# Optimization experiments

Measured on AMD Instinct MI355X. Metric: run time of the kernel, lower is better.

Reference implementation:

```python
import jax, jax.numpy as jnp
import numpy as np

NSAMPLES = [64, 32, 16, 8, 4]
TEMPERATURE = 1.0


def square_distance(src, dst):
    # src [B,N,C], dst [B,M,C] -> [B,N,M]
    d = -2.0 * jnp.einsum('bnc,bmc->bnm', src, dst)
    d = d + jnp.sum(src ** 2, -1)[:, :, None]
    d = d + jnp.sum(dst ** 2, -1)[:, None, :]
    return d


def knn_point(nsample, xyz, new_xyz):
    # indices of nsample nearest points in xyz for each query in new_xyz
    sqrdists = square_distance(new_xyz, xyz)           # [B,S,N]
    _, idx = jax.lax.top_k(-sqrdists, nsample)         # smallest distances
    return idx                                         # [B,S,nsample]


def index_points(points, idx):
    # points [B,N,C], idx [B,S,K] -> [B,S,K,C]
    B, S, K = idx.shape
    flat = idx.reshape(B, S * K)
    out = jnp.take_along_axis(points, flat[..., None], axis=1)
    return out.reshape(B, S, K, points.shape[-1])


def boundary_loss(labels, coords, feats, num_classes):
    onehot = jax.nn.one_hot(labels, num_classes, dtype=jnp.float32)  # [B,N,C]
    loss = jnp.float32(0.0)
    for i, (coord, feat) in enumerate(zip(coords, feats)):
        if i == 0:
            probability_labels = onehot
        else:
            kneighbors = i * 4
            nb_idx = knn_point(kneighbors, coords[0], coord)          # [B,Ni,k]
            probability_labels = index_points(onehot, nb_idx).mean(-2)  # [B,Ni,C]
        nsample = NSAMPLES[i]
        neighbor_indexs = knn_point(nsample, coord, coord)            # [B,Ni,ns]
        neighbor_labels = index_points(probability_labels, neighbor_indexs)  # [B,Ni,ns,C]
        neighbor_feats = index_points(feat, neighbor_indexs)          # [B,Ni,ns,D]
        center_label = jnp.argmax(probability_labels, -1)[:, :, None]  # [B,Ni,1]
        neighbor_label = jnp.argmax(neighbor_labels, -1)               # [B,Ni,ns]
        mask = (center_label == neighbor_label)                        # [B,Ni,ns] bool
        cnt = jnp.sum(mask.astype(jnp.int32), -1)
        point_mask = (cnt > 0) & (cnt < nsample)                       # [B,Ni]
        any_pm = jnp.any(point_mask)
        pm = point_mask.astype(jnp.float32)[:, :, None]                # [B,Ni,1]
        # pairwise feature distances to the nsample neighbors
        diff = feat[:, :, None, :] - neighbor_feats                    # [B,Ni,ns,D]
        dist = jnp.sqrt(jnp.sum(diff ** 2, -1) + 1e-6)                 # [B,Ni,ns]
        dist = -dist
        dist = dist - jnp.max(dist, -1, keepdims=True)
        dist = dist / TEMPERATURE
        exp = jnp.exp(dist)
        pos = jnp.sum(exp * mask.astype(jnp.float32) * pm)
        neg = jnp.sum(exp * pm)
        pos = jnp.where(any_pm, pos, 1.0)
        neg = jnp.where(any_pm, neg, 1.0)
        term = -jnp.log(pos / (neg + 1e-6))
        loss = loss + jnp.where(any_pm, term, 0.0)
    return loss


def setup_inputs() -> dict:
    key = jax.random.key(0)
    ks = jax.random.split(key, 12)
    B, N = 2, 4096
    sizes = [N, N // 4, N // 16, N // 64, N // 256]
    inp = {}
    inp['labels'] = jax.random.randint(ks[0], (B, N), 0, 21)
    for i, s in enumerate(sizes):
        inp[f'coord{i}'] = jax.random.normal(ks[1 + i], (B, s, 3), dtype=jnp.float32)
        inp[f'feat{i}'] = jax.random.normal(ks[6 + i], (B, s, 32), dtype=jnp.float32)
    inp['num_classes'] = 21
    return inp


def reference(labels, coord0, coord1, coord2, coord3, coord4,
              feat0, feat1, feat2, feat3, feat4, num_classes):
    coords = [coord0, coord1, coord2, coord3, coord4]
    feats = [feat0, feat1, feat2, feat3, feat4]
    return boundary_loss(labels, coords, feats, num_classes)
```

## Files before the change

kernel.cpp:

```cpp
#include <hip/hip_runtime.h>
#include <math.h>

#define WAVE 64
#define NC 21

__device__ __forceinline__ unsigned f32_ord(float f) {
    unsigned u = __float_as_uint(f);
    return (u & 0x80000000u) ? ~u : (u | 0x80000000u);
}

__device__ __forceinline__ int wave_red_sum_dpp(int v) {
    v += __builtin_amdgcn_update_dpp(0, v, 0x111, 0xf, 0xf, true);
    v += __builtin_amdgcn_update_dpp(0, v, 0x112, 0xf, 0xf, true);
    v += __builtin_amdgcn_update_dpp(0, v, 0x114, 0xf, 0xf, true);
    v += __builtin_amdgcn_update_dpp(0, v, 0x118, 0xf, 0xf, true);
    v += __builtin_amdgcn_update_dpp(0, v, 0x142, 0xa, 0xf, true);
    v += __builtin_amdgcn_update_dpp(0, v, 0x143, 0xc, 0xf, true);
    return __builtin_amdgcn_readlane(v, 63);
}

__device__ __forceinline__ unsigned wave_min_u32(unsigned v) {
#pragma unroll
    for (int off = 32; off >= 1; off >>= 1) {
        unsigned o = (unsigned)__shfl_xor((int)v, off, WAVE);
        v = (o < v) ? o : v;
    }
    return v;
}

__device__ __forceinline__ unsigned wave_max_u32(unsigned v) {
#pragma unroll
    for (int off = 32; off >= 1; off >>= 1) {
        unsigned o = (unsigned)__shfl_xor((int)v, off, WAVE);
        v = (o > v) ? o : v;
    }
    return v;
}

__device__ __forceinline__ float wave_max_f32(float v) {
#pragma unroll
    for (int off = 32; off >= 1; off >>= 1)
        v = fmaxf(v, __shfl_xor(v, off, WAVE));
    return v;
}

__device__ __forceinline__ float wave_sum_f32(float v) {
#pragma unroll
    for (int off = 32; off >= 1; off >>= 1)
        v += __shfl_xor(v, off, WAVE);
    return v;
}

struct SelShm {
    unsigned long long cand[512];
    int wcnt[4];
    int sel[64];
};

template <int NI, int NS>
__device__ __forceinline__ void block_select_topNS(
    const float* __restrict__ rp,
    float qx, float qy, float qz, float nq,
    SelShm& shm, int tid)
{
    constexpr int SLICE = NI / 4;
    constexpr int NPL = (SLICE >= 64) ? (SLICE / 64) : 1;
    constexpr int CAPX = (NS < 32) ? 32 : NS;
    constexpr int STRIDE = NS + CAPX;
    const int lane = tid & 63;
    const int wid = tid >> 6;
    const int wbase = wid * SLICE;
    const unsigned long long lmask = (1ull << lane) - 1ull;

    unsigned ok[NPL];
#pragma unroll
    for (int j = 0; j < NPL; ++j) {
        unsigned o = 0xFFFFFFFFu;
        int gl = (SLICE >= 64) ? (j * 64 + lane) : lane;
        if (SLICE >= 64 || lane < SLICE) {
            int g = wbase + gl;
            float rx = rp[3*g], ry = rp[3*g+1], rz = rp[3*g+2];
            float nr = rx*rx + ry*ry + rz*rz;
            float dot = qx*rx + qy*ry + qz*rz;
            o = f32_ord(-2.0f*dot + nq + nr);
        }
        ok[j] = o;
    }

    unsigned mn = 0xFFFFFFFFu, mx = 0u;
#pragma unroll
    for (int j = 0; j < NPL; ++j) {
        mn = (ok[j] < mn) ? ok[j] : mn;
        unsigned v = (ok[j] == 0xFFFFFFFFu) ? 0u : ok[j];
        mx = (v > mx) ? v : mx;
    }
    mn = wave_min_u32(mn);
    mx = wave_max_u32(mx);

    unsigned lo = mn, hi = mx;
    int cLo = 0, cHi = SLICE;
    while (lo < hi && (cHi - cLo) > CAPX) {
        unsigned piv = lo + ((hi - lo) >> 1);
        int c = 0;
#pragma unroll
        for (int j = 0; j < NPL; ++j) c += (ok[j] <= piv) ? 1 : 0;
        c = wave_red_sum_dpp(c);
        if (c >= NS) { hi = piv; cHi = c; } else { lo = piv + 1; cLo = c; }
    }

    unsigned long long* cw = shm.cand + wid * STRIDE;
    int wcnt;
    if (lo == hi && (cHi - cLo) > CAPX) {
        unsigned V = lo;
        int off = 0;
#pragma unroll
        for (int j = 0; j < NPL; ++j) {
            bool s = ok[j] < V;
            unsigned long long mk = __ballot(s);
            if (s) {
                int gl = (SLICE >= 64) ? (j*64 + lane) : lane;
                cw[off + __popcll(mk & lmask)] =
                    ((unsigned long long)ok[j] << 32) | (unsigned)(wbase + gl);
            }
            off += __popcll(mk);
        }
        int R = NS - off;
        unsigned consumed = 0u;
        for (int r = 0; r < R; ++r) {
            int bj = -1;
#pragma unroll
            for (int j = NPL - 1; j >= 0; --j)
                if (ok[j] == V && !((consumed >> j) & 1u)) bj = j;
            unsigned g = 0xFFFFFFFFu;
            if (bj >= 0) {
                int gl = (SLICE >= 64) ? (bj*64 + lane) : lane;
                g = (unsigned)(wbase + gl);
            }
            unsigned mg = wave_min_u32(g);
            if (bj >= 0 && g == mg) consumed |= (1u << bj);
            if (lane == 0) cw[off + r] = ((unsigned long long)V << 32) | mg;
        }
        wcnt = NS;
    } else {
        int off = 0;
#pragma unroll
        for (int j = 0; j < NPL; ++j) {
            bool s = ok[j] <= hi;
            unsigned long long mk = __ballot(s);
            if (s) {
                int gl = (SLICE >= 64) ? (j*64 + lane) : lane;
                cw[off + __popcll(mk & lmask)] =
                    ((unsigned long long)ok[j] << 32) | (unsigned)(wbase + gl);
            }
            off += __popcll(mk);
        }
        wcnt = off;
    }
    if (lane == 0) shm.wcnt[wid] = wcnt;
    __syncthreads();

    if (wid == 0) {
        constexpr int CAND = 4 * STRIDE;
        constexpr int NPLC = (CAND + 63) / 64;
        unsigned long long ck[NPLC];
        int w0 = shm.wcnt[0], w1 = shm.wcnt[1], w2 = shm.wcnt[2], w3 = shm.wcnt[3];
#pragma unroll
        for (int i = 0; i < NPLC; ++i) {
            int idx = i * 64 + lane;
            unsigned long long v = ~0ull;
            if (idx < CAND) {
                int w = idx / STRIDE;
                int slot = idx - w * STRIDE;
                int wc = (w == 0) ? w0 : (w == 1) ? w1 : (w == 2) ? w2 : w3;
                if (slot < wc) v = shm.cand[idx];
            }
            ck[i] = v;
        }
        unsigned mn2 = 0xFFFFFFFFu, mx2 = 0u;
#pragma unroll
        for (int i = 0; i < NPLC; ++i) {
            unsigned k = (unsigned)(ck[i] >> 32);
            mn2 = (k < mn2) ? k : mn2;
            unsigned v = (k == 0xFFFFFFFFu) ? 0u : k;
            mx2 = (v > mx2) ? v : mx2;
        }
        mn2 = wave_min_u32(mn2);
        mx2 = wave_max_u32(mx2);
        unsigned lo2 = mn2, hi2 = mx2;
        while (lo2 < hi2) {
            unsigned piv = lo2 + ((hi2 - lo2) >> 1);
            int c = 0;
#pragma unroll
            for (int i = 0; i < NPLC; ++i)
                c += ((unsigned)(ck[i] >> 32) <= piv) ? 1 : 0;
            c = wave_red_sum_dpp(c);
            if (c >= NS) hi2 = piv; else lo2 = piv + 1;
        }
        unsigned V2 = lo2;
        int c2 = 0;
#pragma unroll
        for (int i = 0; i < NPLC; ++i)
            c2 += ((unsigned)(ck[i] >> 32) < V2) ? 1 : 0;
        int clt2 = wave_red_sum_dpp(c2);
        int R2 = NS - clt2;
        int off = 0;
#pragma unroll
        for (int i = 0; i < NPLC; ++i) {
            bool s = ((unsigned)(ck[i] >> 32)) < V2;
            unsigned long long mk = __ballot(s);
            if (s) shm.sel[off + __popcll(mk & lmask)] = (int)(unsigned)ck[i];
            off += __popcll(mk);
        }
        unsigned consumed = 0u;
        for (int r = 0; r < R2; ++r) {
            unsigned bg = 0xFFFFFFFFu; int bi = -1;
#pragma unroll
            for (int i = 0; i < NPLC; ++i) {
                unsigned k = (unsigned)(ck[i] >> 32);
                unsigned g = (unsigned)ck[i];
                if (k == V2 && !((consumed >> i) & 1u) && g < bg) { bg = g; bi = i; }
            }
            unsigned mg = wave_min_u32(bg);
            if (bi >= 0 && bg == mg) consumed |= (1u << bi);
            if (lane == 0) shm.sel[clt2 + r] = (int)mg;
        }
    }
}

template <int NQ, int K>
__device__ __forceinline__ void knn_level(
    const float* __restrict__ qc, const float* __restrict__ rc,
    const int* __restrict__ rl, int* __restrict__ out,
    int qb, SelShm& shm, int tid)
{
    int b = qb / NQ, qi = qb - b * NQ;
    const float* qp = qc + ((long)b * NQ + qi) * 3;
    float qx = qp[0], qy = qp[1], qz = qp[2];
    float nq = qx*qx + qy*qy + qz*qz;
    block_select_topNS<4096, K>(rc + (long)b * 4096 * 3, qx, qy, qz, nq, shm, tid);
    if ((tid >> 6) == 0) {
        int lane = tid & 63;
        int lb = (lane < K) ? rl[(long)b * 4096 + shm.sel[lane]] : -1;
        int cnt = 0;
#pragma unroll
        for (int k = 0; k < K; ++k) {
            int lk = __shfl(lb, k, WAVE);
            cnt += (lk == lane) ? 1 : 0;
        }
        int key = (lane < NC) ? ((cnt << 8) | (255 - lane)) : 0;
#pragma unroll
        for (int off = 32; off >= 1; off >>= 1) {
            int o = __shfl_xor(key, off, WAVE);
            key = (o > key) ? o : key;
        }
        if (lane == 0) out[(long)b * NQ + qi] = 255 - (key & 255);
    }
}

template <int NI, int NS>
__device__ __forceinline__ void boundary_level(
    const float* __restrict__ coord, const float* __restrict__ feat,
    const int* __restrict__ lbl,
    double* __restrict__ pos, double* __restrict__ neg, int* __restrict__ anyf,
    int qb, SelShm& shm, int tid)
{
    int b = qb / NI, qi = qb - b * NI;
    const float* qp = coord + ((long)b * NI + qi) * 3;
    float qx = qp[0], qy = qp[1], qz = qp[2];
    float nq = qx*qx + qy*qy + qz*qz;
    block_select_topNS<NI, NS>(coord + (long)b * NI * 3, qx, qy, qz, nq, shm, tid);
    if ((tid >> 6) == 0) {
        int lane = tid & 63;
        int center = lbl[(long)b * NI + qi];
        bool m = false;
        float dj = -INFINITY;
        if (lane < NS) {
            int nb = shm.sel[lane];
            m = (lbl[(long)b * NI + nb] == center);
            const float4* fq = (const float4*)(feat + ((long)b * NI + qi) * 32);
            const float4* fn = (const float4*)(feat + ((long)b * NI + nb) * 32);
            float s = 0.f;
#pragma unroll
            for (int d = 0; d < 8; ++d) {
                float4 a = fq[d], c = fn[d];
                float d0 = a.x - c.x, d1 = a.y - c.y;
                float d2 = a.z - c.z, d3 = a.w - c.w;
                s += d0*d0 + d1*d1 + d2*d2 + d3*d3;
            }
            dj = -sqrtf(s + 1e-6f);
        }
        unsigned long long mb = __ballot(m);
        int cnt = __popcll(mb);
        float mxv = wave_max_f32(dj);
        float ej = 0.f, pj = 0.f;
        if (lane < NS) {
            ej = expf(dj - mxv);
            pj = m ? ej : 0.f;
        }
        float se = wave_sum_f32(ej);
        float sp = wave_sum_f32(pj);
        bool pm = (cnt > 0) && (cnt < NS);
        if (pm && lane == 0) {
            atomicAdd(pos, (double)sp);
            atomicAdd(neg, (double)se);
            *anyf = 1;
        }
    }
}

__global__ __launch_bounds__(256) void knn_fused(
    const float* __restrict__ c1, const float* __restrict__ c2,
    const float* __restrict__ c3, const float* __restrict__ c4,
    const float* __restrict__ c0, const int* __restrict__ labels,
    int* __restrict__ lbl1, int* __restrict__ lbl2,
    int* __restrict__ lbl3, int* __restrict__ lbl4,
    double* __restrict__ posA, double* __restrict__ negA,
    int* __restrict__ anyA, int B)
{
    __shared__ SelShm shm;
    int blk = blockIdx.x, tid = threadIdx.x;
    int n1 = B * 1024, n2 = n1 + B * 256, n3 = n2 + B * 64, n4 = n3 + B * 16;
    if (blk < n1)      knn_level<1024, 4>(c1, c0, labels, lbl1, blk,      shm, tid);
    else if (blk < n2) knn_level<256,  8>(c2, c0, labels, lbl2, blk - n1, shm, tid);
    else if (blk < n3) knn_level<64,  12>(c3, c0, labels, lbl3, blk - n2, shm, tid);
    else if (blk < n4) knn_level<16,  16>(c4, c0, labels, lbl4, blk - n3, shm, tid);
    else if (tid < 5) { posA[tid] = 0.0; negA[tid] = 0.0; anyA[tid] = 0; }
}

__global__ __launch_bounds__(256) void boundary_fused(
    const float* __restrict__ c0, const float* __restrict__ c1,
    const float* __restrict__ c2, const float* __restrict__ c3,
    const float* __restrict__ c4,
    const float* __restrict__ f0, const float* __restrict__ f1,
    const float* __restrict__ f2, const float* __restrict__ f3,
    const float* __restrict__ f4,
    const int* __restrict__ labels, const int* __restrict__ lbl1,
    const int* __restrict__ lbl2, const int* __restrict__ lbl3,
    const int* __restrict__ lbl4,
    double* __restrict__ posA, double* __restrict__ negA,
    int* __restrict__ anyA, int B)
{
    __shared__ SelShm shm;
    int blk = blockIdx.x, tid = threadIdx.x;
    int m0 = B * 4096, m1 = m0 + B * 1024, m2 = m1 + B * 256;
    int m3 = m2 + B * 64, m4 = m3 + B * 16;
    if (blk < m0)
        boundary_level<4096, 64>(c0, f0, labels, posA+0, negA+0, anyA+0, blk,      shm, tid);
    else if (blk < m1)
        boundary_level<1024, 32>(c1, f1, lbl1,   posA+1, negA+1, anyA+1, blk - m0, shm, tid);
    else if (blk < m2)
        boundary_level<256,  16>(c2, f2, lbl2,   posA+2, negA+2, anyA+2, blk - m1, shm, tid);
    else if (blk < m3)
        boundary_level<64,    8>(c3, f3, lbl3,   posA+3, negA+3, anyA+3, blk - m2, shm, tid);
    else if (blk < m4)
        boundary_level<16,    4>(c4, f4, lbl4,   posA+4, negA+4, anyA+4, blk - m3, shm, tid);
}

__global__ void finalize_kernel(const double* __restrict__ pos,
                                const double* __restrict__ neg,
                                const int* __restrict__ anyf,
                                float* __restrict__ out) {
    if (threadIdx.x == 0 && blockIdx.x == 0) {
        float loss = 0.f;
        for (int i = 0; i < 5; ++i) {
            if (anyf[i]) {
                float p = (float)pos[i];
                float n = (float)neg[i];
                loss += -logf(p / (n + 1e-6f));
            }
        }
        out[0] = loss;
    }
}

extern "C" void kernel_launch(void* const* d_in, const int* in_sizes, int n_in,
                              void* d_out, int out_size, void* d_ws, size_t ws_size,
                              hipStream_t stream) {
    (void)out_size; (void)ws_size;
    const int* labels = (const int*)d_in[0];
    const float* coord[5];
    const float* feat[5];
    bool interleaved = (n_in >= 3 && in_sizes[2] == 2 * 4096 * 32);
    if (interleaved) {
        for (int i = 0; i < 5; ++i) {
            coord[i] = (const float*)d_in[1 + 2 * i];
            feat[i]  = (const float*)d_in[2 + 2 * i];
        }
    } else {
        for (int i = 0; i < 5; ++i) {
            coord[i] = (const float*)d_in[1 + i];
            feat[i]  = (const float*)d_in[6 + i];
        }
    }
    int B = in_sizes[0] / 4096;

    double* posA = (double*)d_ws;
    double* negA = posA + 5;
    int* anyA = (int*)(negA + 5);
    int* lbl1 = anyA + 8;
    int* lbl2 = lbl1 + B * 1024;
    int* lbl3 = lbl2 + B * 256;
    int* lbl4 = lbl3 + B * 64;

    int knn_grid = B * (1024 + 256 + 64 + 16) + 1;
    hipLaunchKernelGGL(knn_fused, dim3(knn_grid), dim3(256), 0, stream,
                       coord[1], coord[2], coord[3], coord[4],
                       coord[0], labels, lbl1, lbl2, lbl3, lbl4,
                       posA, negA, anyA, B);

    int bnd_grid = B * (4096 + 1024 + 256 + 64 + 16);
    hipLaunchKernelGGL(boundary_fused, dim3(bnd_grid), dim3(256), 0, stream,
                       coord[0], coord[1], coord[2], coord[3], coord[4],
                       feat[0], feat[1], feat[2], feat[3], feat[4],
                       labels, lbl1, lbl2, lbl3, lbl4,
                       posA, negA, anyA, B);

    hipLaunchKernelGGL(finalize_kernel, dim3(1), dim3(1), 0, stream,
                       posA, negA, anyA, (float*)d_out);
}
```

Baseline: 391.6 us.

## Replace bisection top-k selection with 4-pass radix histogram select

The per-wave bisection on distance keys followed by a second candidate-merge pass in one wave is replaced with a block-wide 8-bit radix select. Each pass builds shared-memory histograms with atomics, and one wave scans them to find the k-th key. Selected indices are then written with an atomic counter, and ties are broken with a block-wide min loop. This removes the serial bisection iterations and the single-wave merge stage. In exchange it adds LDS atomics, several __syncthreads per pass, and a per-tie block barrier loop.

```diff
diff --git a/kernel.cpp b/kernel.cpp
--- a/kernel.cpp
+++ b/kernel.cpp
@@ -9,16 +9,6 @@
     return (u & 0x80000000u) ? ~u : (u | 0x80000000u);
 }
 
-__device__ __forceinline__ int wave_red_sum_dpp(int v) {
-    v += __builtin_amdgcn_update_dpp(0, v, 0x111, 0xf, 0xf, true);
-    v += __builtin_amdgcn_update_dpp(0, v, 0x112, 0xf, 0xf, true);
-    v += __builtin_amdgcn_update_dpp(0, v, 0x114, 0xf, 0xf, true);
-    v += __builtin_amdgcn_update_dpp(0, v, 0x118, 0xf, 0xf, true);
-    v += __builtin_amdgcn_update_dpp(0, v, 0x142, 0xa, 0xf, true);
-    v += __builtin_amdgcn_update_dpp(0, v, 0x143, 0xc, 0xf, true);
-    return __builtin_amdgcn_readlane(v, 63);
-}
-
 __device__ __forceinline__ unsigned wave_min_u32(unsigned v) {
 #pragma unroll
     for (int off = 32; off >= 1; off >>= 1) {
@@ -28,15 +18,6 @@
     return v;
 }
 
-__device__ __forceinline__ unsigned wave_max_u32(unsigned v) {
-#pragma unroll
-    for (int off = 32; off >= 1; off >>= 1) {
-        unsigned o = (unsigned)__shfl_xor((int)v, off, WAVE);
-        v = (o > v) ? o : v;
-    }
-    return v;
-}
-
 __device__ __forceinline__ float wave_max_f32(float v) {
 #pragma unroll
     for (int off = 32; off >= 1; off >>= 1)
@@ -52,10 +33,42 @@
 }
 
 struct SelShm {
-    unsigned long long cand[512];
-    int wcnt[4];
+    int hist[4][256];
     int sel[64];
+    int swave[4];
+    int scnt;
 };
+
+__device__ __forceinline__ void radix_scan_step(SelShm& shm, int lane,
+                                                int& need, unsigned& Vhi) {
+    int i0 = 4 * lane;
+    int b0 = shm.hist[0][i0]   + shm.hist[1][i0]   + shm.hist[2][i0]   + shm.hist[3][i0];
+    int b1 = shm.hist[0][i0+1] + shm.hist[1][i0+1] + shm.hist[2][i0+1] + shm.hist[3][i0+1];
+    int b2 = shm.hist[0][i0+2] + shm.hist[1][i0+2] + shm.hist[2][i0+2] + shm.hist[3][i0+2];
+    int b3 = shm.hist[0][i0+3] + shm.hist[1][i0+3] + shm.hist[2][i0+3] + shm.hist[3][i0+3];
+    int lsum = b0 + b1 + b2 + b3;
+    int c = lsum;
+#pragma unroll
+    for (int off = 1; off < 64; off <<= 1) {
+        int o = __shfl_up(c, off, WAVE);
+        c += (lane >= off) ? o : 0;
+    }
+    unsigned long long mball = __ballot(c >= need);
+    int Ls = __ffsll((unsigned long long)mball) - 1;
+    int cL = __shfl(c, Ls, WAVE);
+    int lsumL = __shfl(lsum, Ls, WAVE);
+    int B0 = __shfl(b0, Ls, WAVE);
+    int B1 = __shfl(b1, Ls, WAVE);
+    int B2 = __shfl(b2, Ls, WAVE);
+    int e = cL - lsumL;
+    int T;
+    if (e + B0 >= need)                { T = 4 * Ls + 0; }
+    else if (e + B0 + B1 >= need)      { T = 4 * Ls + 1; e += B0; }
+    else if (e + B0 + B1 + B2 >= need) { T = 4 * Ls + 2; e += B0 + B1; }
+    else                               { T = 4 * Ls + 3; e += B0 + B1 + B2; }
+    need -= e;
+    Vhi = (Vhi << 8) | (unsigned)T;
+}
 
 template <int NI, int NS>
 __device__ __forceinline__ void block_select_topNS(
@@ -63,22 +76,18 @@
     float qx, float qy, float qz, float nq,
     SelShm& shm, int tid)
 {
-    constexpr int SLICE = NI / 4;
-    constexpr int NPL = (SLICE >= 64) ? (SLICE / 64) : 1;
-    constexpr int CAPX = (NS < 32) ? 32 : NS;
-    constexpr int STRIDE = NS + CAPX;
+    constexpr int NPL = (NI + 255) / 256;
+    constexpr bool FULL = (NPL * 256 == NI);
     const int lane = tid & 63;
     const int wid = tid >> 6;
-    const int wbase = wid * SLICE;
     const unsigned long long lmask = (1ull << lane) - 1ull;
 
     unsigned ok[NPL];
 #pragma unroll
     for (int j = 0; j < NPL; ++j) {
+        int g = j * 256 + tid;
         unsigned o = 0xFFFFFFFFu;
-        int gl = (SLICE >= 64) ? (j * 64 + lane) : lane;
-        if (SLICE >= 64 || lane < SLICE) {
-            int g = wbase + gl;
+        if (FULL || g < NI) {
             float rx = rp[3*g], ry = rp[3*g+1], rz = rp[3*g+2];
             float nr = rx*rx + ry*ry + rz*rz;
             float dot = qx*rx + qy*ry + qz*rz;
@@ -87,143 +96,78 @@
         ok[j] = o;
     }
 
-    unsigned mn = 0xFFFFFFFFu, mx = 0u;
+    int* hf = &shm.hist[0][0];
+#pragma unroll
+    for (int i = 0; i < 4; ++i) hf[i * 256 + tid] = 0;
+    if (tid == 0) shm.scnt = 0;
+    __syncthreads();
+
+    int need = NS;
+    unsigned Vhi = 0;
+
+#pragma unroll
+    for (int j = 0; j < NPL; ++j)
+        atomicAdd(&shm.hist[wid][ok[j] >> 24], 1);
+    __syncthreads();
+    radix_scan_step(shm, lane, need, Vhi);
+    __syncthreads();
+#pragma unroll
+    for (int i = 0; i < 4; ++i) hf[i * 256 + tid] = 0;
+    __syncthreads();
+
+#pragma unroll
+    for (int pass = 1; pass < 4; ++pass) {
+        const int shift = 24 - 8 * pass;
+#pragma unroll
+        for (int j = 0; j < NPL; ++j) {
+            if ((ok[j] >> (shift + 8)) == Vhi)
+                atomicAdd(&shm.hist[wid][(ok[j] >> shift) & 255], 1);
+        }
+        __syncthreads();
+        radix_scan_step(shm, lane, need, Vhi);
+        __syncthreads();
+        if (pass < 3) {
+#pragma unroll
+            for (int i = 0; i < 4; ++i) hf[i * 256 + tid] = 0;
+            __syncthreads();
+        }
+    }
+
+    const unsigned V = Vhi;
+    const int R = need;
+    const int clt = NS - R;
+
 #pragma unroll
     for (int j = 0; j < NPL; ++j) {
-        mn = (ok[j] < mn) ? ok[j] : mn;
-        unsigned v = (ok[j] == 0xFFFFFFFFu) ? 0u : ok[j];
-        mx = (v > mx) ? v : mx;
-    }
-    mn = wave_min_u32(mn);
-    mx = wave_max_u32(mx);
-
-    unsigned lo = mn, hi = mx;
-    int cLo = 0, cHi = SLICE;
-    while (lo < hi && (cHi - cLo) > CAPX) {
-        unsigned piv = lo + ((hi - lo) >> 1);
-        int c = 0;
-#pragma unroll
-        for (int j = 0; j < NPL; ++j) c += (ok[j] <= piv) ? 1 : 0;
-        c = wave_red_sum_dpp(c);
-        if (c >= NS) { hi = piv; cHi = c; } else { lo = piv + 1; cLo = c; }
-    }
-
-    unsigned long long* cw = shm.cand + wid * STRIDE;
-    int wcnt;
-    if (lo == hi && (cHi - cLo) > CAPX) {
-        unsigned V = lo;
-        int off = 0;
-#pragma unroll
-        for (int j = 0; j < NPL; ++j) {
-            bool s = ok[j] < V;
-            unsigned long long mk = __ballot(s);
-            if (s) {
-                int gl = (SLICE >= 64) ? (j*64 + lane) : lane;
-                cw[off + __popcll(mk & lmask)] =
-                    ((unsigned long long)ok[j] << 32) | (unsigned)(wbase + gl);
-            }
-            off += __popcll(mk);
-        }
-        int R = NS - off;
-        unsigned consumed = 0u;
-        for (int r = 0; r < R; ++r) {
-            int bj = -1;
-#pragma unroll
-            for (int j = NPL - 1; j >= 0; --j)
-                if (ok[j] == V && !((consumed >> j) & 1u)) bj = j;
-            unsigned g = 0xFFFFFFFFu;
-            if (bj >= 0) {
-                int gl = (SLICE >= 64) ? (bj*64 + lane) : lane;
-                g = (unsigned)(wbase + gl);
-            }
-            unsigned mg = wave_min_u32(g);
-            if (bj >= 0 && g == mg) consumed |= (1u << bj);
-            if (lane == 0) cw[off + r] = ((unsigned long long)V << 32) | mg;
-        }
-        wcnt = NS;
-    } else {
-        int off = 0;
-#pragma unroll
-        for (int j = 0; j < NPL; ++j) {
-            bool s = ok[j] <= hi;
-            unsigned long long mk = __ballot(s);
-            if (s) {
-                int gl = (SLICE >= 64) ? (j*64 + lane) : lane;
-                cw[off + __popcll(mk & lmask)] =
-                    ((unsigned long long)ok[j] << 32) | (unsigned)(wbase + gl);
-            }
-            off += __popcll(mk);
-        }
-        wcnt = off;
-    }
-    if (lane == 0) shm.wcnt[wid] = wcnt;
-    __syncthreads();
-
-    if (wid == 0) {
-        constexpr int CAND = 4 * STRIDE;
-        constexpr int NPLC = (CAND + 63) / 64;
-        unsigned long long ck[NPLC];
-        int w0 = shm.wcnt[0], w1 = shm.wcnt[1], w2 = shm.wcnt[2], w3 = shm.wcnt[3];
-#pragma unroll
-        for (int i = 0; i < NPLC; ++i) {
-            int idx = i * 64 + lane;
-            unsigned long long v = ~0ull;
-            if (idx < CAND) {
-                int w = idx / STRIDE;
-                int slot = idx - w * STRIDE;
-                int wc = (w == 0) ? w0 : (w == 1) ? w1 : (w == 2) ? w2 : w3;
-                if (slot < wc) v = shm.cand[idx];
-            }
-            ck[i] = v;
-        }
-        unsigned mn2 = 0xFFFFFFFFu, mx2 = 0u;
-#pragma unroll
-        for (int i = 0; i < NPLC; ++i) {
-            unsigned k = (unsigned)(ck[i] >> 32);
-            mn2 = (k < mn2) ? k : mn2;
-            unsigned v = (k == 0xFFFFFFFFu) ? 0u : k;
-            mx2 = (v > mx2) ? v : mx2;
-        }
-        mn2 = wave_min_u32(mn2);
-        mx2 = wave_max_u32(mx2);
-        unsigned lo2 = mn2, hi2 = mx2;
-        while (lo2 < hi2) {
-            unsigned piv = lo2 + ((hi2 - lo2) >> 1);
-            int c = 0;
-#pragma unroll
-            for (int i = 0; i < NPLC; ++i)
-                c += ((unsigned)(ck[i] >> 32) <= piv) ? 1 : 0;
-            c = wave_red_sum_dpp(c);
-            if (c >= NS) hi2 = piv; else lo2 = piv + 1;
-        }
-        unsigned V2 = lo2;
-        int c2 = 0;
-#pragma unroll
-        for (int i = 0; i < NPLC; ++i)
-            c2 += ((unsigned)(ck[i] >> 32) < V2) ? 1 : 0;
-        int clt2 = wave_red_sum_dpp(c2);
-        int R2 = NS - clt2;
-        int off = 0;
-#pragma unroll
-        for (int i = 0; i < NPLC; ++i) {
-            bool s = ((unsigned)(ck[i] >> 32)) < V2;
-            unsigned long long mk = __ballot(s);
-            if (s) shm.sel[off + __popcll(mk & lmask)] = (int)(unsigned)ck[i];
-            off += __popcll(mk);
-        }
-        unsigned consumed = 0u;
-        for (int r = 0; r < R2; ++r) {
-            unsigned bg = 0xFFFFFFFFu; int bi = -1;
-#pragma unroll
-            for (int i = 0; i < NPLC; ++i) {
-                unsigned k = (unsigned)(ck[i] >> 32);
-                unsigned g = (unsigned)ck[i];
-                if (k == V2 && !((consumed >> i) & 1u) && g < bg) { bg = g; bi = i; }
-            }
-            unsigned mg = wave_min_u32(bg);
-            if (bi >= 0 && bg == mg) consumed |= (1u << bi);
-            if (lane == 0) shm.sel[clt2 + r] = (int)mg;
-        }
+        bool s = ok[j] < V;
+        unsigned long long mk = __ballot(s);
+        int n = __popcll(mk);
+        if (n) {
+            int wb = 0;
+            if (lane == 0) wb = atomicAdd(&shm.scnt, n);
+            wb = __shfl(wb, 0, WAVE);
+            if (s) shm.sel[wb + __popcll(mk & lmask)] = j * 256 + tid;
+        }
+    }
+
+    unsigned consumed = 0u;
+    for (int r = 0; r < R; ++r) {
+        int bj = -1;
+#pragma unroll
+        for (int j = NPL - 1; j >= 0; --j)
+            if (ok[j] == V && !((consumed >> j) & 1u)) bj = j;
+        unsigned g = (bj >= 0) ? (unsigned)(bj * 256 + tid) : 0xFFFFFFFFu;
+        unsigned mg = wave_min_u32(g);
+        if (lane == 0) shm.swave[wid] = (int)mg;
+        __syncthreads();
+        unsigned t0 = (unsigned)shm.swave[0], t1 = (unsigned)shm.swave[1];
+        unsigned t2 = (unsigned)shm.swave[2], t3 = (unsigned)shm.swave[3];
+        unsigned ta = (t0 < t1) ? t0 : t1;
+        unsigned tb = (t2 < t3) ? t2 : t3;
+        unsigned t = (ta < tb) ? ta : tb;
+        if (bj >= 0 && g == t) consumed |= (1u << bj);
+        if (tid == 0) shm.sel[clt + r] = (int)t;
+        __syncthreads();
     }
 }
 
```

Result: slower. 448.8 us (+14.6%).
